# Performance work log

Measured on AMD Instinct MI355X. Metric: run time of the kernel, lower is better.

## Reference

```python
import jax, jax.numpy as jnp
import numpy as np

D_K = 8192   # sequence length (module calls it d_k)
D_MODEL = 128

def setup_inputs() -> dict:
    key = jax.random.key(0)
    k1, k2, k3 = jax.random.split(key, 3)
    Q = jax.random.normal(k1, (D_K, D_MODEL), dtype=jnp.float32)
    K = jax.random.normal(k2, (D_K, D_MODEL), dtype=jnp.float32)
    V = jax.random.normal(k3, (D_K, D_MODEL), dtype=jnp.float32)
    return {"Q": Q, "K": K, "V": V}

def reference(Q, K, V):
    # scores: [d_k, d_k] -- full attention matrix, scaled by 1/sqrt(d_k)
    # (faithful to the source: scale uses d_k, the sequence dim)
    inv_scale = 1.0 / jnp.sqrt(jnp.asarray(D_K, dtype=Q.dtype))
    scores = jnp.einsum('qd,kd->qk', Q, K) * inv_scale
    attn = jax.nn.softmax(scores, axis=-1)
    return jnp.einsum('qk,kd->qd', attn, V)
```

## Files before the change

### kernel.cpp

```cpp
#include <hip/hip_runtime.h>

#define SEQ 8192
#define DM  128

typedef __attribute__((ext_vector_type(8)))  short bf16x8;
typedef __attribute__((ext_vector_type(16))) float f32x16;

static __device__ __forceinline__ unsigned short f2bf(float f) {
    unsigned int u = __builtin_bit_cast(unsigned int, f);
    u += 0x7FFFu + ((u >> 16) & 1u);
    return (unsigned short)(u >> 16);
}
static __device__ __forceinline__ unsigned int pack2bf(float a, float b) {
    return ((unsigned int)f2bf(b) << 16) | (unsigned int)f2bf(a);
}
static __device__ __forceinline__ bf16x8 as_frag(uint4 v) {
    return __builtin_bit_cast(bf16x8, v);
}
static __device__ __forceinline__ unsigned int pack2bf_trunc(float a, float b) {
    return __builtin_amdgcn_perm(__builtin_bit_cast(unsigned int, b),
                                 __builtin_bit_cast(unsigned int, a), 0x07060302u);
}

static __device__ __forceinline__ void gl_lds16(const void* g, void* l) {
    __builtin_amdgcn_global_load_lds(
        (const __attribute__((address_space(1))) void*)(unsigned long long)g,
        (__attribute__((address_space(3))) void*)(unsigned int)(unsigned long long)l,
        16, 0, 0);
}

#define CL2 (1.4426950408889634f / 90.50966799187809f)

__global__ __launch_bounds__(256) void prep_kernel(
        const float* __restrict__ Q, const float* __restrict__ K,
        const float* __restrict__ V,
        unsigned short* __restrict__ Qb, unsigned short* __restrict__ Kb,
        unsigned short* __restrict__ VT) {
    __shared__ unsigned short tile[32][33];
    int bx = blockIdx.x;
    if (bx < 2048) {
        int t = bx * 256 + threadIdx.x;
        const int n4 = SEQ * DM / 4;
        if (t < n4) {
            float4 v = ((const float4*)Q)[t];
            ((uint2*)Qb)[t] = make_uint2(pack2bf(v.x * CL2, v.y * CL2),
                                         pack2bf(v.z * CL2, v.w * CL2));
        } else {
            float4 v = ((const float4*)K)[t - n4];
            ((uint2*)Kb)[t - n4] = make_uint2(pack2bf(v.x, v.y), pack2bf(v.z, v.w));
        }
    } else {
        int bid = bx - 2048;
        int k0 = (bid & 255) * 32, d0 = (bid >> 8) * 32;
        int tx = threadIdx.x & 31, ty = threadIdx.x >> 5;
        #pragma unroll
        for (int i = 0; i < 32; i += 8) {
            float v = V[(size_t)(k0 + ty + i) * DM + d0 + tx];
            tile[tx][ty + i] = f2bf(v);
        }
        __syncthreads();
        #pragma unroll
        for (int i = 0; i < 32; i += 8)
            VT[(size_t)(d0 + ty + i) * SEQ + k0 + tx] = tile[ty + i][tx];
    }
}

__global__ __launch_bounds__(512, 2) void attn_kernel(
        const unsigned short* __restrict__ Qb,
        const unsigned short* __restrict__ Kb,
        const unsigned short* __restrict__ VT,
        float* __restrict__ Opart, float* __restrict__ Lpart) {
    __shared__ __align__(16) char smem[68096];
    const int tid  = threadIdx.x;
    const int wid  = tid >> 6;
    const int lane = tid & 63;
    const int i    = wid & 3;
    const int j    = wid >> 2;
    const int q    = lane & 31;
    const int h    = lane >> 5;
    const int qt   = blockIdx.x & 63;
    const int ks   = blockIdx.x >> 6;
    const int qbase   = qt * 128 + i * 32;
    const int keybase = ks * 2048 + j * 1024;

    uint4 qf[8];
    {
        const unsigned short* qrow = Qb + (qbase + q) * DM + 8 * h;
        #pragma unroll
        for (int s = 0; s < 8; ++s) qf[s] = *(const uint4*)(qrow + 16 * s);
    }

    f32x16 oacc[4];
    #pragma unroll
    for (int mb = 0; mb < 4; ++mb)
        #pragma unroll
        for (int r = 0; r < 16; ++r) oacc[mb][r] = 0.f;
    float lsum = 0.f;

    char* const mybuf0 = smem + j * 32768;
    auto stage = [&](int b, int key0) {
        char* base = mybuf0 + b * 16384;
        #pragma unroll
        for (int u = 0; u < 2; ++u) {
            int ki = i * 2 + u;
            {
                int L = ki * 64 + lane;
                int r = L >> 4, cp = L & 15, cl = cp ^ (r & 7);
                gl_lds16(Kb + (key0 + r) * DM + cl * 8, base + ki * 1024);
            }
            {
                int L = ki * 64 + lane;
                int rd = L >> 2, cp = L & 3, cl = cp ^ (rd & 3);
                gl_lds16(VT + (size_t)rd * SEQ + key0 + cl * 8,
                         base + 8192 + ki * 1024);
            }
        }
    };

    stage(0, keybase);
    #pragma unroll 1
    for (int t = 0; t < 32; ++t) {
        __syncthreads();
        if (t < 31) stage((t + 1) & 1, keybase + (t + 1) * 32);
        const char* kb = mybuf0 + (t & 1) * 16384;
        const char* vb = kb + 8192;

        uint4 kf[8];
        #pragma unroll
        for (int s = 0; s < 8; ++s) {
            int cp = (2 * s + h) ^ (q & 7);
            kf[s] = *(const uint4*)(kb + q * 256 + cp * 16);
        }
        f32x16 sacc;
        #pragma unroll
        for (int r = 0; r < 16; ++r) sacc[r] = 0.f;
        #pragma unroll
        for (int s = 0; s < 8; ++s)
            sacc = __builtin_amdgcn_mfma_f32_32x32x16_bf16(
                       as_frag(kf[s]), as_frag(qf[s]), sacc, 0, 0, 0);

        uint4 vf[8];
        #pragma unroll
        for (int mb = 0; mb < 4; ++mb)
            #pragma unroll
            for (int st = 0; st < 2; ++st) {
                int dd = 32 * mb + q;
                int cp = (2 * st + h) ^ (q & 3);
                vf[mb * 2 + st] = *(const uint4*)(vb + dd * 64 + cp * 16);
            }

        float p[16];
        #pragma unroll
        for (int r = 0; r < 16; ++r) {
            p[r] = __builtin_amdgcn_exp2f(sacc[r]);
            lsum += p[r];
        }
        unsigned int pk[8], px[8];
        #pragma unroll
        for (int jj = 0; jj < 8; ++jj) pk[jj] = pack2bf_trunc(p[2 * jj], p[2 * jj + 1]);
        #pragma unroll
        for (int jj = 0; jj < 8; ++jj) px[jj] = (unsigned int)__shfl_xor((int)pk[jj], 32);
        uint4 B0, B1;
        B0.x = h ? px[2] : pk[0];  B0.y = h ? px[3] : pk[1];
        B0.z = h ? pk[2] : px[0];  B0.w = h ? pk[3] : px[1];
        B1.x = h ? px[6] : pk[4];  B1.y = h ? px[7] : pk[5];
        B1.z = h ? pk[6] : px[4];  B1.w = h ? pk[7] : px[5];

        #pragma unroll
        for (int mb = 0; mb < 4; ++mb) {
            oacc[mb] = __builtin_amdgcn_mfma_f32_32x32x16_bf16(
                           as_frag(vf[mb * 2 + 0]), as_frag(B0), oacc[mb], 0, 0, 0);
            oacc[mb] = __builtin_amdgcn_mfma_f32_32x32x16_bf16(
                           as_frag(vf[mb * 2 + 1]), as_frag(B1), oacc[mb], 0, 0, 0);
        }
    }

    float l2 = lsum + __shfl_xor(lsum, 32);
    float* Lx = (float*)(smem + 67584);
    __syncthreads();
    float* L0 = (float*)(smem + i * 16896);
    if (j == 0) {
        #pragma unroll
        for (int mb = 0; mb < 4; ++mb)
            #pragma unroll
            for (int r = 0; r < 16; ++r) {
                int dl = 32 * mb + (r & 3) + 8 * (r >> 2) + 4 * h;
                L0[dl * 33 + q] = oacc[mb][r];
            }
        if (h == 0) Lx[i * 32 + q] = l2;
    }
    __syncthreads();
    if (j == 1) {
        #pragma unroll
        for (int mb = 0; mb < 4; ++mb)
            #pragma unroll
            for (int r = 0; r < 16; ++r) {
                int dl = 32 * mb + (r & 3) + 8 * (r >> 2) + 4 * h;
                L0[dl * 33 + q] += oacc[mb][r];
            }
        if (h == 0) Lpart[(size_t)ks * SEQ + qbase + q] = Lx[i * 32 + q] + l2;
    }
    __syncthreads();
    #pragma unroll
    for (int u = 0; u < 8; ++u) {
        int idx = u * 512 + tid;
        int row = idx >> 5, c4 = idx & 31;
        int ig = row >> 5, qq = row & 31;
        const float* Ls = (const float*)(smem + ig * 16896);
        float4 v;
        v.x = Ls[(c4 * 4 + 0) * 33 + qq];
        v.y = Ls[(c4 * 4 + 1) * 33 + qq];
        v.z = Ls[(c4 * 4 + 2) * 33 + qq];
        v.w = Ls[(c4 * 4 + 3) * 33 + qq];
        size_t orow = (size_t)ks * SEQ + qt * 128 + row;
        ((float4*)Opart)[orow * 32 + c4] = v;
    }
}

__global__ __launch_bounds__(256) void reduce_kernel(
        const float* __restrict__ Opart, const float* __restrict__ Lpart,
        float* __restrict__ Out) {
    int t = blockIdx.x * 256 + threadIdx.x;
    int row = t >> 5;
    float L = Lpart[row] + Lpart[SEQ + row] + Lpart[2 * SEQ + row] + Lpart[3 * SEQ + row];
    const float4* O4 = (const float4*)Opart;
    const size_t stride = (size_t)SEQ * 32;
    float4 a = O4[t], b = O4[stride + t], c = O4[2 * stride + t], d = O4[3 * stride + t];
    float r = 1.0f / L;
    float4 o;
    o.x = (a.x + b.x + c.x + d.x) * r;
    o.y = (a.y + b.y + c.y + d.y) * r;
    o.z = (a.z + b.z + c.z + d.z) * r;
    o.w = (a.w + b.w + c.w + d.w) * r;
    ((float4*)Out)[t] = o;
}

extern "C" void kernel_launch(void* const* d_in, const int* in_sizes, int n_in,
                              void* d_out, int out_size, void* d_ws, size_t ws_size,
                              hipStream_t stream) {
    const float* Q = (const float*)d_in[0];
    const float* K = (const float*)d_in[1];
    const float* V = (const float*)d_in[2];
    char* ws = (char*)d_ws;
    unsigned short* Qb = (unsigned short*)ws;
    unsigned short* Kb = (unsigned short*)(ws + 2 * 1024 * 1024);
    unsigned short* VT = (unsigned short*)(ws + 4 * 1024 * 1024);
    float* Opart = (float*)(ws + 6 * 1024 * 1024);
    float* Lpart = (float*)(ws + 22 * 1024 * 1024);
    float* Out = (float*)d_out;

    prep_kernel<<<3072, 256, 0, stream>>>(Q, K, V, Qb, Kb, VT);
    attn_kernel<<<256, 512, 0, stream>>>(Qb, Kb, VT, Opart, Lpart);
    reduce_kernel<<<1024, 256, 0, stream>>>(Opart, Lpart, Out);
}
```

Before: 122.2 us.

## Pre-swizzle K/V into MFMA fragment tiles, double key splits, bf16 partials

The prep kernel now writes K and V in a per-tile layout that matches the MFMA fragment order, fused into one 256-block pass. Each lane in the attention loop can then stage and read 16-byte chunks contiguously, with no XOR swizzle or address arithmetic. The key dimension is split across 8 partitions instead of 4, doubling the grid to 512 blocks for better occupancy across CUs. Partial outputs are stored as bf16 in a transposed layout, and the reduction goes through shared memory to cut partial-buffer traffic, at some cost in precision. The unpadded LDS reads in the epilogue may introduce bank conflicts.

```diff
diff --git a/kernel.cpp b/kernel.cpp
--- a/kernel.cpp
+++ b/kernel.cpp
@@ -2,6 +2,7 @@
 
 #define SEQ 8192
 #define DM  128
+#define KS  8
 
 typedef __attribute__((ext_vector_type(8)))  short bf16x8;
 typedef __attribute__((ext_vector_type(16))) float f32x16;
@@ -14,6 +15,12 @@
 static __device__ __forceinline__ unsigned int pack2bf(float a, float b) {
     return ((unsigned int)f2bf(b) << 16) | (unsigned int)f2bf(a);
 }
+static __device__ __forceinline__ float bflo(unsigned int u) {
+    return __builtin_bit_cast(float, u << 16);
+}
+static __device__ __forceinline__ float bfhi(unsigned int u) {
+    return __builtin_bit_cast(float, u & 0xFFFF0000u);
+}
 static __device__ __forceinline__ bf16x8 as_frag(uint4 v) {
     return __builtin_bit_cast(bf16x8, v);
 }
@@ -21,67 +28,79 @@
     return __builtin_amdgcn_perm(__builtin_bit_cast(unsigned int, b),
                                  __builtin_bit_cast(unsigned int, a), 0x07060302u);
 }
-
 static __device__ __forceinline__ void gl_lds16(const void* g, void* l) {
     __builtin_amdgcn_global_load_lds(
         (const __attribute__((address_space(1))) void*)(unsigned long long)g,
         (__attribute__((address_space(3))) void*)(unsigned int)(unsigned long long)l,
         16, 0, 0);
 }
-
 #define CL2 (1.4426950408889634f / 90.50966799187809f)
 
 __global__ __launch_bounds__(256) void prep_kernel(
         const float* __restrict__ Q, const float* __restrict__ K,
         const float* __restrict__ V,
-        unsigned short* __restrict__ Qb, unsigned short* __restrict__ Kb,
-        unsigned short* __restrict__ VT) {
-    __shared__ unsigned short tile[32][33];
-    int bx = blockIdx.x;
-    if (bx < 2048) {
-        int t = bx * 256 + threadIdx.x;
-        const int n4 = SEQ * DM / 4;
-        if (t < n4) {
-            float4 v = ((const float4*)Q)[t];
-            ((uint2*)Qb)[t] = make_uint2(pack2bf(v.x * CL2, v.y * CL2),
-                                         pack2bf(v.z * CL2, v.w * CL2));
-        } else {
-            float4 v = ((const float4*)K)[t - n4];
-            ((uint2*)Kb)[t - n4] = make_uint2(pack2bf(v.x, v.y), pack2bf(v.z, v.w));
-        }
-    } else {
-        int bid = bx - 2048;
-        int k0 = (bid & 255) * 32, d0 = (bid >> 8) * 32;
-        int tx = threadIdx.x & 31, ty = threadIdx.x >> 5;
-        #pragma unroll
-        for (int i = 0; i < 32; i += 8) {
-            float v = V[(size_t)(k0 + ty + i) * DM + d0 + tx];
-            tile[tx][ty + i] = f2bf(v);
-        }
-        __syncthreads();
-        #pragma unroll
-        for (int i = 0; i < 32; i += 8)
-            VT[(size_t)(d0 + ty + i) * SEQ + k0 + tx] = tile[ty + i][tx];
+        uint2* __restrict__ Qb2, uint4* __restrict__ Kt, uint4* __restrict__ Vt) {
+    __shared__ float VL[32 * 132 + 4];
+    const int b = blockIdx.x, tid = threadIdx.x;
+    const float4* Q4 = (const float4*)Q;
+    const float4* K4 = (const float4*)K;
+    const float4* V4 = (const float4*)V;
+
+    #pragma unroll
+    for (int u = 0; u < 4; ++u) {
+        int f4 = u * 256 + tid;
+        int k = f4 >> 5, c4 = f4 & 31;
+        float4 v = V4[(size_t)b * 1024 + f4];
+        *(float4*)(VL + k * 132 + c4 * 4) = v;
+    }
+    #pragma unroll
+    for (int u = 0; u < 4; ++u) {
+        int f4 = u * 256 + tid;
+        float4 v = Q4[(size_t)b * 1024 + f4];
+        Qb2[(size_t)b * 1024 + f4] = make_uint2(pack2bf(v.x * CL2, v.y * CL2),
+                                                pack2bf(v.z * CL2, v.w * CL2));
+    }
+    #pragma unroll
+    for (int u = 0; u < 2; ++u) {
+        int p = u * 256 + tid;
+        int q = p & 31, h = (p >> 5) & 1, s = p >> 6;
+        int fi = ((size_t)0, (b * 32 + q) * 32 + s * 4 + h * 2);
+        float4 a = K4[fi], c = K4[fi + 1];
+        Kt[(size_t)b * 512 + p] = make_uint4(pack2bf(a.x, a.y), pack2bf(a.z, a.w),
+                                             pack2bf(c.x, c.y), pack2bf(c.z, c.w));
+    }
+    __syncthreads();
+    #pragma unroll
+    for (int u = 0; u < 2; ++u) {
+        int p = u * 256 + tid;
+        int q = p & 31, h = (p >> 5) & 1, w = p >> 6;
+        int d = (w >> 1) * 32 + q;
+        int k0 = (w & 1) * 16 + h * 8;
+        unsigned int r[4];
+        #pragma unroll
+        for (int jj = 0; jj < 4; ++jj) {
+            float e0 = VL[(k0 + 2 * jj) * 132 + d];
+            float e1 = VL[(k0 + 2 * jj + 1) * 132 + d];
+            r[jj] = pack2bf(e0, e1);
+        }
+        Vt[(size_t)b * 512 + p] = make_uint4(r[0], r[1], r[2], r[3]);
     }
 }
 
 __global__ __launch_bounds__(512, 2) void attn_kernel(
         const unsigned short* __restrict__ Qb,
-        const unsigned short* __restrict__ Kb,
-        const unsigned short* __restrict__ VT,
-        float* __restrict__ Opart, float* __restrict__ Lpart) {
-    __shared__ __align__(16) char smem[68096];
-    const int tid  = threadIdx.x;
-    const int wid  = tid >> 6;
-    const int lane = tid & 63;
-    const int i    = wid & 3;
-    const int j    = wid >> 2;
-    const int q    = lane & 31;
-    const int h    = lane >> 5;
-    const int qt   = blockIdx.x & 63;
-    const int ks   = blockIdx.x >> 6;
-    const int qbase   = qt * 128 + i * 32;
-    const int keybase = ks * 2048 + j * 1024;
+        const uint4* __restrict__ Kt,
+        const uint4* __restrict__ Vt,
+        uint2* __restrict__ Opart, float* __restrict__ Lpart) {
+    __shared__ __align__(16) char smem[65536];
+    __shared__ float Lx[128];
+    const int tid = threadIdx.x;
+    const int wid = tid >> 6, lane = tid & 63;
+    const int i = wid & 3, j = wid >> 2;
+    const int q = lane & 31, h = lane >> 5;
+    const int qt = blockIdx.x & 63, ks = blockIdx.x >> 6;
+    const int qbase = qt * 128 + i * 32;
+    const int tile0 = ks * 32 + j * 16;
 
     uint4 qf[8];
     {
@@ -97,40 +116,30 @@
         for (int r = 0; r < 16; ++r) oacc[mb][r] = 0.f;
     float lsum = 0.f;
 
-    char* const mybuf0 = smem + j * 32768;
-    auto stage = [&](int b, int key0) {
-        char* base = mybuf0 + b * 16384;
+    char* const mybuf = smem + j * 32768;
+    auto stage = [&](int buf, int tile) {
+        char* base = mybuf + buf * 16384;
+        const uint4* kt = Kt + (size_t)tile * 512;
+        const uint4* vt = Vt + (size_t)tile * 512;
         #pragma unroll
         for (int u = 0; u < 2; ++u) {
             int ki = i * 2 + u;
-            {
-                int L = ki * 64 + lane;
-                int r = L >> 4, cp = L & 15, cl = cp ^ (r & 7);
-                gl_lds16(Kb + (key0 + r) * DM + cl * 8, base + ki * 1024);
-            }
-            {
-                int L = ki * 64 + lane;
-                int rd = L >> 2, cp = L & 3, cl = cp ^ (rd & 3);
-                gl_lds16(VT + (size_t)rd * SEQ + key0 + cl * 8,
-                         base + 8192 + ki * 1024);
-            }
+            gl_lds16(kt + ki * 64 + lane, base + ki * 1024);
+            gl_lds16(vt + ki * 64 + lane, base + 8192 + ki * 1024);
         }
     };
 
-    stage(0, keybase);
+    stage(0, tile0);
     #pragma unroll 1
-    for (int t = 0; t < 32; ++t) {
+    for (int t = 0; t < 16; ++t) {
         __syncthreads();
-        if (t < 31) stage((t + 1) & 1, keybase + (t + 1) * 32);
-        const char* kb = mybuf0 + (t & 1) * 16384;
-        const char* vb = kb + 8192;
+        if (t < 15) stage((t + 1) & 1, tile0 + t + 1);
+        const char* kl = mybuf + (t & 1) * 16384 + lane * 16;
 
         uint4 kf[8];
         #pragma unroll
-        for (int s = 0; s < 8; ++s) {
-            int cp = (2 * s + h) ^ (q & 7);
-            kf[s] = *(const uint4*)(kb + q * 256 + cp * 16);
-        }
+        for (int s = 0; s < 8; ++s) kf[s] = *(const uint4*)(kl + s * 1024);
+
         f32x16 sacc;
         #pragma unroll
         for (int r = 0; r < 16; ++r) sacc[r] = 0.f;
@@ -141,13 +150,7 @@
 
         uint4 vf[8];
         #pragma unroll
-        for (int mb = 0; mb < 4; ++mb)
-            #pragma unroll
-            for (int st = 0; st < 2; ++st) {
-                int dd = 32 * mb + q;
-                int cp = (2 * st + h) ^ (q & 3);
-                vf[mb * 2 + st] = *(const uint4*)(vb + dd * 64 + cp * 16);
-            }
+        for (int w = 0; w < 8; ++w) vf[w] = *(const uint4*)(kl + 8192 + w * 1024);
 
         float p[16];
         #pragma unroll
@@ -176,16 +179,15 @@
     }
 
     float l2 = lsum + __shfl_xor(lsum, 32);
-    float* Lx = (float*)(smem + 67584);
-    __syncthreads();
-    float* L0 = (float*)(smem + i * 16896);
+    __syncthreads();
+    float* Lg = (float*)(smem + i * 16384);
     if (j == 0) {
         #pragma unroll
         for (int mb = 0; mb < 4; ++mb)
             #pragma unroll
             for (int r = 0; r < 16; ++r) {
                 int dl = 32 * mb + (r & 3) + 8 * (r >> 2) + 4 * h;
-                L0[dl * 33 + q] = oacc[mb][r];
+                Lg[dl * 32 + q] = oacc[mb][r];
             }
         if (h == 0) Lx[i * 32 + q] = l2;
     }
@@ -196,7 +198,7 @@
             #pragma unroll
             for (int r = 0; r < 16; ++r) {
                 int dl = 32 * mb + (r & 3) + 8 * (r >> 2) + 4 * h;
-                L0[dl * 33 + q] += oacc[mb][r];
+                Lg[dl * 32 + q] += oacc[mb][r];
             }
         if (h == 0) Lpart[(size_t)ks * SEQ + qbase + q] = Lx[i * 32 + q] + l2;
     }
@@ -204,35 +206,56 @@
     #pragma unroll
     for (int u = 0; u < 8; ++u) {
         int idx = u * 512 + tid;
-        int row = idx >> 5, c4 = idx & 31;
-        int ig = row >> 5, qq = row & 31;
-        const float* Ls = (const float*)(smem + ig * 16896);
-        float4 v;
-        v.x = Ls[(c4 * 4 + 0) * 33 + qq];
-        v.y = Ls[(c4 * 4 + 1) * 33 + qq];
-        v.z = Ls[(c4 * 4 + 2) * 33 + qq];
-        v.w = Ls[(c4 * 4 + 3) * 33 + qq];
-        size_t orow = (size_t)ks * SEQ + qt * 128 + row;
-        ((float4*)Opart)[orow * 32 + c4] = v;
+        int rd = idx >> 5, c4 = idx & 31;
+        int ig = c4 >> 3, q4 = c4 & 7;
+        float4 v = *(const float4*)(smem + ig * 16384 + (rd * 8 + q4) * 16);
+        Opart[(((size_t)(ks * 64 + qt)) * 128 + rd) * 32 + c4] =
+            make_uint2(pack2bf(v.x, v.y), pack2bf(v.z, v.w));
     }
 }
 
 __global__ __launch_bounds__(256) void reduce_kernel(
-        const float* __restrict__ Opart, const float* __restrict__ Lpart,
+        const uint2* __restrict__ Opart, const float* __restrict__ Lpart,
         float* __restrict__ Out) {
-    int t = blockIdx.x * 256 + threadIdx.x;
-    int row = t >> 5;
-    float L = Lpart[row] + Lpart[SEQ + row] + Lpart[2 * SEQ + row] + Lpart[3 * SEQ + row];
-    const float4* O4 = (const float4*)Opart;
-    const size_t stride = (size_t)SEQ * 32;
-    float4 a = O4[t], b = O4[stride + t], c = O4[2 * stride + t], d = O4[3 * stride + t];
-    float r = 1.0f / L;
-    float4 o;
-    o.x = (a.x + b.x + c.x + d.x) * r;
-    o.y = (a.y + b.y + c.y + d.y) * r;
-    o.z = (a.z + b.z + c.z + d.z) * r;
-    o.w = (a.w + b.w + c.w + d.w) * r;
-    ((float4*)Out)[t] = o;
+    __shared__ float T[32 * 132 + 4];
+    __shared__ float Rinv[128];
+    const int tid = threadIdx.x;
+    const int qt = blockIdx.x & 63, dq = blockIdx.x >> 6;
+    if (tid < 128) {
+        float L = 0.f;
+        #pragma unroll
+        for (int ks = 0; ks < KS; ++ks) L += Lpart[(size_t)ks * SEQ + qt * 128 + tid];
+        Rinv[tid] = 1.0f / L;
+    }
+    const int c = tid & 31, dsub = tid >> 5;
+    float4 acc[4];
+    #pragma unroll
+    for (int rr = 0; rr < 4; ++rr) { acc[rr].x = acc[rr].y = acc[rr].z = acc[rr].w = 0.f; }
+    #pragma unroll 1
+    for (int ks = 0; ks < KS; ++ks) {
+        #pragma unroll
+        for (int rr = 0; rr < 4; ++rr) {
+            int d_l = rr * 8 + dsub;
+            uint2 w = Opart[(((size_t)(ks * 64 + qt)) * 128 + dq * 32 + d_l) * 32 + c];
+            acc[rr].x += bflo(w.x); acc[rr].y += bfhi(w.x);
+            acc[rr].z += bflo(w.y); acc[rr].w += bfhi(w.y);
+        }
+    }
+    #pragma unroll
+    for (int rr = 0; rr < 4; ++rr)
+        *(float4*)(T + (rr * 8 + dsub) * 132 + c * 4) = acc[rr];
+    __syncthreads();
+    const int q_l = tid >> 1, hf = tid & 1;
+    float r = Rinv[q_l];
+    #pragma unroll
+    for (int g = 0; g < 4; ++g) {
+        float4 o;
+        o.x = T[(hf * 16 + g * 4 + 0) * 132 + q_l] * r;
+        o.y = T[(hf * 16 + g * 4 + 1) * 132 + q_l] * r;
+        o.z = T[(hf * 16 + g * 4 + 2) * 132 + q_l] * r;
+        o.w = T[(hf * 16 + g * 4 + 3) * 132 + q_l] * r;
+        *(float4*)(Out + ((size_t)(qt * 128 + q_l)) * DM + dq * 32 + hf * 16 + g * 4) = o;
+    }
 }
 
 extern "C" void kernel_launch(void* const* d_in, const int* in_sizes, int n_in,
@@ -242,14 +265,15 @@
     const float* K = (const float*)d_in[1];
     const float* V = (const float*)d_in[2];
     char* ws = (char*)d_ws;
-    unsigned short* Qb = (unsigned short*)ws;
-    unsigned short* Kb = (unsigned short*)(ws + 2 * 1024 * 1024);
-    unsigned short* VT = (unsigned short*)(ws + 4 * 1024 * 1024);
-    float* Opart = (float*)(ws + 6 * 1024 * 1024);
-    float* Lpart = (float*)(ws + 22 * 1024 * 1024);
-    float* Out = (float*)d_out;
-
-    prep_kernel<<<3072, 256, 0, stream>>>(Q, K, V, Qb, Kb, VT);
-    attn_kernel<<<256, 512, 0, stream>>>(Qb, Kb, VT, Opart, Lpart);
-    reduce_kernel<<<1024, 256, 0, stream>>>(Opart, Lpart, Out);
-}
+    uint2* Qb2  = (uint2*)ws;
+    uint4* Kt   = (uint4*)(ws + 2 * 1024 * 1024);
+    uint4* Vt   = (uint4*)(ws + 4 * 1024 * 1024);
+    float* Lpart= (float*)(ws + 6 * 1024 * 1024);
+    uint2* Opart= (uint2*)(ws + 6 * 1024 * 1024 + 262144);
+    float* Out  = (float*)d_out;
+
+    prep_kernel<<<256, 256, 0, stream>>>(Q, K, V, Qb2, Kt, Vt);
+    attn_kernel<<<512, 512, 0, stream>>>((const unsigned short*)Qb2, Kt, Vt,
+                                         Opart, Lpart);
+    reduce_kernel<<<256, 256, 0, stream>>>(Opart, Lpart, Out);
+}
```

Result: faster. 117.0 us (-4.2%).
